# Performance work log

Hardware: AMD Instinct MI355X
Metric: run time of the kernel (lower is better)

The kernel has to match this reference:

```python
import jax, jax.numpy as jnp
import numpy as np

B, T, I, H, O = 128, 1024, 512, 1024, 512
LN_EPS = 1e-5

def _linear_params(key, out_dim, in_dim):
    k1, k2 = jax.random.split(key)
    bound = 1.0 / np.sqrt(in_dim)
    W = jax.random.uniform(k1, (out_dim, in_dim), jnp.float32, -bound, bound)
    b = jax.random.uniform(k2, (out_dim,), jnp.float32, -bound, bound)
    return W, b

def setup_inputs() -> dict:
    key = jax.random.key(0)
    ks = jax.random.split(key, 10)
    x = jax.random.normal(ks[0], (B, T, I), jnp.float32)
    Wir, bir = _linear_params(ks[1], H, I)
    Whr, bhr = _linear_params(ks[2], H, H)
    Wiz, biz = _linear_params(ks[3], H, I)
    Whz, bhz = _linear_params(ks[4], H, H)
    Win, bin_ = _linear_params(ks[5], H, I)
    Whn, bhn = _linear_params(ks[6], H, H)
    Wskip, bskip = _linear_params(ks[7], H, I)
    gamma = jnp.ones((H,), jnp.float32)
    beta = jnp.zeros((H,), jnp.float32)
    Wout, bout = _linear_params(ks[8], O, H)
    return dict(x=x, Wir=Wir, bir=bir, Whr=Whr, bhr=bhr, Wiz=Wiz, biz=biz,
                Whz=Whz, bhz=bhz, Win=Win, bin_=bin_, Whn=Whn, bhn=bhn,
                Wskip=Wskip, bskip=bskip, gamma=gamma, beta=beta,
                Wout=Wout, bout=bout)

def reference(x, Wir, bir, Whr, bhr, Wiz, biz, Whz, bhz, Win, bin_, Whn, bhn,
              Wskip, bskip, gamma, beta, Wout, bout):
    # Precompute input-side projections in one batched GEMM each (same math as per-step Linear).
    rx = jnp.einsum('bti,hi->bth', x, Wir) + bir  # (B,T,H)
    zx = jnp.einsum('bti,hi->bth', x, Wiz) + biz
    nx = jnp.einsum('bti,hi->bth', x, Win) + bin_

    def step(h, inp):
        rx_t, zx_t, nx_t = inp
        r = jax.nn.sigmoid(rx_t + h @ Whr.T + bhr)
        z = jax.nn.sigmoid(zx_t + h @ Whz.T + bhz)
        n = jnp.tanh(nx_t + r * (h @ Whn.T + bhn))
        h_new = (1.0 - z) * n + z * h
        return h_new, h_new

    h0 = jnp.zeros((x.shape[0], Whr.shape[0]), x.dtype)
    xs = (jnp.swapaxes(rx, 0, 1), jnp.swapaxes(zx, 0, 1), jnp.swapaxes(nx, 0, 1))
    _, hs = jax.lax.scan(step, h0, xs)  # hs: (T,B,H)
    hs = jnp.swapaxes(hs, 0, 1)  # (B,T,H)

    skip = jnp.einsum('bti,hi->bth', x, Wskip) + bskip
    combined = hs + skip
    mu = jnp.mean(combined, axis=-1, keepdims=True)
    var = jnp.var(combined, axis=-1, keepdims=True)
    normed = (combined - mu) * jax.lax.rsqrt(var + LN_EPS) * gamma + beta
    out = jnp.einsum('bth,oh->bto', normed, Wout) + bout  # (B,T,O)
    return out
```

## Files before the change

kernel.cpp:

```cpp
#include <hip/hip_runtime.h>

#define T_DIM 1024
#define B_DIM 128
#define I_DIM 512
#define H_DIM 1024
#define O_DIM 512
#define TC 64
#define NCHUNK (T_DIM / TC)

typedef _Float16 half8 __attribute__((ext_vector_type(8)));
typedef _Float16 half4v __attribute__((ext_vector_type(4)));
typedef float floatx4 __attribute__((ext_vector_type(4)));
typedef unsigned int uint4v __attribute__((ext_vector_type(4)));

__device__ __forceinline__ void gload_lds16(const void* g, void* l) {
  __builtin_amdgcn_global_load_lds(
      (const __attribute__((address_space(1))) void*)g,
      (__attribute__((address_space(3))) void*)l, 16, 0, 0);
}

__device__ __forceinline__ float sigmoidf_(float x) {
  return 1.f / (1.f + __expf(-x));
}
__device__ __forceinline__ float tanhf_(float x) {
  float e = __expf(fminf(-2.f * x, 60.f));
  return (1.f - e) / (1.f + e);
}

__global__ __launch_bounds__(256) void k_cvt(const float* __restrict__ s,
                                             _Float16* __restrict__ d, int n4) {
  int i = blockIdx.x * 256 + threadIdx.x;
  if (i < n4) {
    float4 v = ((const float4*)s)[i];
    half4v h = {(_Float16)v.x, (_Float16)v.y, (_Float16)v.z, (_Float16)v.w};
    ((half4v*)d)[i] = h;
  }
}

__global__ __launch_bounds__(256) void k_cvt_x(const float* __restrict__ x,
                                               _Float16* __restrict__ x16, int t0) {
  int i = blockIdx.x * 256 + threadIdx.x;
  int i4 = i & 127;
  int row = i >> 7;
  int b = row & 127, tl = row >> 7;
  float4 v = ((const float4*)(x + ((size_t)b * T_DIM + t0 + tl) * I_DIM))[i4];
  half4v h = {(_Float16)v.x, (_Float16)v.y, (_Float16)v.z, (_Float16)v.w};
  ((half4v*)(x16 + (size_t)row * I_DIM))[i4] = h;
}

__global__ __launch_bounds__(256) void build_bcat(const float* __restrict__ a,
                                                  const float* __restrict__ b,
                                                  const float* __restrict__ c,
                                                  const float* __restrict__ d,
                                                  float* __restrict__ o) {
  int i = blockIdx.x * 256 + threadIdx.x;
  if (i < 4096) {
    const float* p = (i < 1024) ? a : (i < 2048) ? b : (i < 3072) ? c : d;
    o[i] = p[i & 1023];
  }
}

template <int MODE>
__global__ __launch_bounds__(256) void gemm_f16(
    const _Float16* __restrict__ A, const _Float16* __restrict__ B,
    const float* __restrict__ bias, _Float16* __restrict__ C16,
    float* __restrict__ C32, int M, int N, int K, int t0) {
  __shared__ __align__(16) _Float16 As[128 * 64];
  __shared__ __align__(16) _Float16 Bs[128 * 64];
  const int tid = threadIdx.x, lane = tid & 63, wv = tid >> 6;
  const int wm = wv >> 1, wn = wv & 1;
  const int lj = lane & 15, lk = lane >> 4;
  const size_t rowA0 = (size_t)blockIdx.y * 128, colB0 = (size_t)blockIdx.x * 128;
  floatx4 acc[4][4] = {};
  for (int kb = 0; kb < K; kb += 64) {
    __syncthreads();
#pragma unroll
    for (int i = 0; i < 4; ++i) {
      int q = i * 256 + tid;
      int r = q >> 3, c = q & 7;
      gload_lds16(A + (rowA0 + r) * (size_t)K + kb + c * 8, As + (size_t)(i * 4 + wv) * 512);
    }
#pragma unroll
    for (int i = 0; i < 4; ++i) {
      int q = i * 256 + tid;
      int r = q >> 3, c = q & 7;
      gload_lds16(B + (colB0 + r) * (size_t)K + kb + c * 8, Bs + (size_t)(i * 4 + wv) * 512);
    }
    __syncthreads();
#pragma unroll
    for (int ks = 0; ks < 2; ++ks) {
      half8 af[4], bf[4];
#pragma unroll
      for (int am = 0; am < 4; ++am)
        af[am] = *(const half8*)(As + (wm * 64 + am * 16 + lj) * 64 + ks * 32 + lk * 8);
#pragma unroll
      for (int bn = 0; bn < 4; ++bn)
        bf[bn] = *(const half8*)(Bs + (wn * 64 + bn * 16 + lj) * 64 + ks * 32 + lk * 8);
#pragma unroll
      for (int am = 0; am < 4; ++am)
#pragma unroll
        for (int bn = 0; bn < 4; ++bn)
          acc[am][bn] = __builtin_amdgcn_mfma_f32_16x16x32_f16(af[am], bf[bn], acc[am][bn], 0, 0, 0);
    }
  }
#pragma unroll
  for (int am = 0; am < 4; ++am)
#pragma unroll
    for (int bn = 0; bn < 4; ++bn)
#pragma unroll
      for (int rr = 0; rr < 4; ++rr) {
        size_t grow = rowA0 + wm * 64 + am * 16 + lk * 4 + rr;
        size_t gcol = colB0 + wn * 64 + bn * 16 + lj;
        float v = acc[am][bn][rr] + bias[gcol];
        if constexpr (MODE == 0) {
          C16[grow * (size_t)N + gcol] = (_Float16)v;
        } else {
          size_t tl = grow >> 7, b = grow & 127;
          C32[b * (size_t)(T_DIM * O_DIM) + (t0 + tl) * (size_t)O_DIM + gcol] = v;
        }
      }
}

__global__ __launch_bounds__(384) void scan_kernel(
    const _Float16* __restrict__ rznx,
    const _Float16* __restrict__ Whcat,
    const float* __restrict__ bhr, const float* __restrict__ bhz,
    const float* __restrict__ bhn,
    _Float16* __restrict__ h16,
    float* __restrict__ h32,
    _Float16* __restrict__ hs16,
    int* __restrict__ flags,
    int chunk) {
  __shared__ __align__(16) _Float16 hlds[16 * 1024];
  __shared__ float exch[2][2][16 * 17];
  __shared__ __align__(16) _Float16 hout[16][32];
  const int tid = threadIdx.x, lane = tid & 63, wv = tid >> 6;
  const int g = wv % 3, jh = wv / 3;
  const int bg = blockIdx.x & 7, js = blockIdx.x >> 3;
  const int b0 = bg * 16;
  const int jbase = js * 32 + jh * 16;
  const int lj = lane & 15, lk = lane >> 4;
  const int jcol = jbase + lj;

  half8 wf[32];
  {
    const _Float16* wb = Whcat + ((size_t)g * 1024 + jcol) * 1024 + lk * 8;
#pragma unroll
    for (int ks = 0; ks < 32; ++ks) wf[ks] = *(const half8*)(wb + ks * 32);
  }
  const float* bh = (g == 0) ? bhr : (g == 1) ? bhz : bhn;
  const float biasg = bh[jcol];
  float hown[4];
  if (g == 1) {
#pragma unroll
    for (int r = 0; r < 4; ++r) hown[r] = h32[(size_t)(b0 + lk * 4 + r) * 1024 + jcol];
  }
  int cur = 0;
  for (int t = 0; t < TC; ++t) {
    const int gs = chunk * TC + t;
    const _Float16* xg = rznx + ((size_t)t * 128 + b0) * 4096 + g * 1024 + jcol;
    float xv[4];
#pragma unroll
    for (int r = 0; r < 4; ++r) xv[r] = (float)xg[(size_t)(lk * 4 + r) * 4096];
    float nxv[4];
    if (g == 1) {
#pragma unroll
      for (int r = 0; r < 4; ++r)
        nxv[r] = (float)rznx[((size_t)t * 128 + b0 + lk * 4 + r) * 4096 + 2048 + jcol];
    }
    if (tid < 256) {
      const _Float16* hsrc = h16 + (size_t)cur * (128 * 1024) + (size_t)b0 * 1024;
      uint4v vv[8];
      const char* ap[8];
#pragma unroll
      for (int i = 0; i < 8; ++i) {
        int q = tid + i * 256;
        int b = q >> 7, c = q & 127;
        ap[i] = (const char*)(hsrc + b * 1024 + c * 8);
      }
#pragma unroll
      for (int i = 0; i < 8; ++i)
        asm volatile("global_load_dwordx4 %0, %1, off sc0 sc1"
                     : "=v"(vv[i]) : "v"(ap[i]));
      asm volatile("s_waitcnt vmcnt(0)" ::: "memory");
#pragma unroll
      for (int i = 0; i < 8; ++i) {
        int q = tid + i * 256;
        int b = q >> 7, c = q & 127;
        *(uint4v*)((char*)hlds + b * 2048 + ((c ^ (b & 7)) * 16)) = vv[i];
      }
    }
    __syncthreads();
    floatx4 acc = {0.f, 0.f, 0.f, 0.f};
#pragma unroll
    for (int ks = 0; ks < 32; ++ks) {
      int c = ks * 4 + lk;
      int b = lj;
      half8 af = *(const half8*)((const char*)hlds + b * 2048 + ((c ^ (b & 7)) * 16));
      acc = __builtin_amdgcn_mfma_f32_16x16x32_f16(af, wf[ks], acc, 0, 0, 0);
    }
    float zv[4] = {0.f, 0.f, 0.f, 0.f};
    if (g == 0) {
#pragma unroll
      for (int r = 0; r < 4; ++r)
        exch[jh][0][(lk * 4 + r) * 17 + lj] = sigmoidf_(acc[r] + biasg + xv[r]);
    } else if (g == 2) {
#pragma unroll
      for (int r = 0; r < 4; ++r)
        exch[jh][1][(lk * 4 + r) * 17 + lj] = acc[r] + biasg;
    } else {
#pragma unroll
      for (int r = 0; r < 4; ++r) zv[r] = sigmoidf_(acc[r] + biasg + xv[r]);
    }
    __syncthreads();
    if (g == 1) {
#pragma unroll
      for (int r = 0; r < 4; ++r) {
        float rr = exch[jh][0][(lk * 4 + r) * 17 + lj];
        float np = exch[jh][1][(lk * 4 + r) * 17 + lj];
        float n = tanhf_(nxv[r] + rr * np);
        float hn = (1.f - zv[r]) * n + zv[r] * hown[r];
        hown[r] = hn;
        hout[lk * 4 + r][jh * 16 + lj] = (_Float16)hn;
      }
    }
    __syncthreads();
    if (wv == 0) {
      int row = lane >> 2, c = lane & 3;
      uint4v hv = *(const uint4v*)((const char*)hout + row * 64 + c * 16);
      char* p1 = (char*)(h16 + (size_t)(cur ^ 1) * (128 * 1024) +
                         (size_t)(b0 + row) * 1024 + js * 32 + c * 8);
      asm volatile("global_store_dwordx4 %0, %1, off sc0 sc1"
                   :: "v"(p1), "v"(hv) : "memory");
      _Float16* p2 = hs16 + ((size_t)t * 128 + b0 + row) * 1024 + js * 32 + c * 8;
      *(uint4v*)p2 = hv;
      asm volatile("s_waitcnt vmcnt(0)" ::: "memory");
      if (lane == 0) {
        int* fp = flags + ((size_t)bg * 32 + js) * 32;
        int val = gs + 1;
        asm volatile("global_store_dword %0, %1, off sc0 sc1"
                     :: "v"(fp), "v"(val) : "memory");
      }
    } else if (wv == 5) {
      const int* fp = flags + ((size_t)bg * 32 + (lane & 31)) * 32;
      const int target = gs + 1;
      int spin = 0;
      while (true) {
        int v;
        asm volatile("global_load_dword %0, %1, off sc0 sc1\n\ts_waitcnt vmcnt(0)"
                     : "=v"(v) : "v"(fp) : "memory");
        if (__all(v >= target)) break;
        __builtin_amdgcn_s_sleep(1);
        if (++spin > (1 << 17)) break;
      }
    }
    __syncthreads();
    cur ^= 1;
  }
  if (g == 1) {
#pragma unroll
    for (int r = 0; r < 4; ++r) h32[(size_t)(b0 + lk * 4 + r) * 1024 + jcol] = hown[r];
  }
}

__global__ __launch_bounds__(256) void ln_kernel(
    const _Float16* __restrict__ hs, const _Float16* __restrict__ rz,
    const float* __restrict__ gamma, const float* __restrict__ beta,
    _Float16* __restrict__ outp) {
  const int row = blockIdx.x, tid = threadIdx.x;
  const int lane = tid & 63, wv = tid >> 6;
  half4v hv = *(const half4v*)(hs + (size_t)row * 1024 + tid * 4);
  half4v sv = *(const half4v*)(rz + (size_t)row * 4096 + 3072 + tid * 4);
  float v[4];
  float s = 0.f, s2 = 0.f;
#pragma unroll
  for (int j = 0; j < 4; ++j) {
    v[j] = (float)hv[j] + (float)sv[j];
    s += v[j];
    s2 += v[j] * v[j];
  }
#pragma unroll
  for (int o = 32; o > 0; o >>= 1) {
    s += __shfl_xor(s, o, 64);
    s2 += __shfl_xor(s2, o, 64);
  }
  __shared__ float ps[4][2];
  if (lane == 0) { ps[wv][0] = s; ps[wv][1] = s2; }
  __syncthreads();
  s = ps[0][0] + ps[1][0] + ps[2][0] + ps[3][0];
  s2 = ps[0][1] + ps[1][1] + ps[2][1] + ps[3][1];
  const float mu = s * (1.f / 1024.f);
  const float var = s2 * (1.f / 1024.f) - mu * mu;
  const float rstd = rsqrtf(var + 1e-5f);
  half4v ov;
#pragma unroll
  for (int j = 0; j < 4; ++j)
    ov[j] = (_Float16)((v[j] - mu) * rstd * gamma[tid * 4 + j] + beta[tid * 4 + j]);
  *(half4v*)(outp + (size_t)row * 1024 + tid * 4) = ov;
}

extern "C" void kernel_launch(void* const* d_in, const int* in_sizes, int n_in,
                              void* d_out, int out_size, void* d_ws, size_t ws_size,
                              hipStream_t stream) {
  const float* x     = (const float*)d_in[0];
  const float* Wir   = (const float*)d_in[1];
  const float* bir   = (const float*)d_in[2];
  const float* Whr   = (const float*)d_in[3];
  const float* bhr   = (const float*)d_in[4];
  const float* Wiz   = (const float*)d_in[5];
  const float* biz   = (const float*)d_in[6];
  const float* Whz   = (const float*)d_in[7];
  const float* bhz   = (const float*)d_in[8];
  const float* Win   = (const float*)d_in[9];
  const float* bin_  = (const float*)d_in[10];
  const float* Whn   = (const float*)d_in[11];
  const float* bhn   = (const float*)d_in[12];
  const float* Wskip = (const float*)d_in[13];
  const float* bskip = (const float*)d_in[14];
  const float* gamma = (const float*)d_in[15];
  const float* beta  = (const float*)d_in[16];
  const float* Wout  = (const float*)d_in[17];
  const float* bout  = (const float*)d_in[18];
  float* out = (float*)d_out;

  char* ws = (char*)d_ws;
  size_t off = 0;
  auto alloc = [&](size_t bytes) -> char* {
    char* p = ws + off;
    off += (bytes + 255) & ~(size_t)255;
    return p;
  };
  _Float16* x16    = (_Float16*)alloc((size_t)TC * 128 * 512 * 2);
  _Float16* Wcat   = (_Float16*)alloc((size_t)4096 * 512 * 2);
  _Float16* Whcat  = (_Float16*)alloc((size_t)3072 * 1024 * 2);
  _Float16* Wout16 = (_Float16*)alloc((size_t)512 * 1024 * 2);
  float*    bcat   = (float*)alloc(4096 * 4);
  _Float16* rznx   = (_Float16*)alloc((size_t)TC * 128 * 4096 * 2);
  _Float16* h16    = (_Float16*)alloc((size_t)2 * 128 * 1024 * 2);
  float*    h32    = (float*)alloc((size_t)128 * 1024 * 4);
  _Float16* hs16   = (_Float16*)alloc((size_t)TC * 128 * 1024 * 2);
  _Float16* normed = (_Float16*)alloc((size_t)TC * 128 * 1024 * 2);
  int*      flags  = (int*)alloc(8 * 32 * 32 * sizeof(int));

  k_cvt<<<512, 256, 0, stream>>>(Wir, Wcat + 0 * 524288, 131072);
  k_cvt<<<512, 256, 0, stream>>>(Wiz, Wcat + 1 * 524288, 131072);
  k_cvt<<<512, 256, 0, stream>>>(Win, Wcat + 2 * 524288, 131072);
  k_cvt<<<512, 256, 0, stream>>>(Wskip, Wcat + 3 * 524288, 131072);
  k_cvt<<<1024, 256, 0, stream>>>(Whr, Whcat + 0 * 1048576, 262144);
  k_cvt<<<1024, 256, 0, stream>>>(Whz, Whcat + 1 * 1048576, 262144);
  k_cvt<<<1024, 256, 0, stream>>>(Whn, Whcat + 2 * 1048576, 262144);
  k_cvt<<<512, 256, 0, stream>>>(Wout, Wout16, 131072);
  build_bcat<<<16, 256, 0, stream>>>(bir, biz, bin_, bskip, bcat);
  hipMemsetAsync(h16, 0, (size_t)2 * 128 * 1024 * 2, stream);
  hipMemsetAsync(h32, 0, (size_t)128 * 1024 * 4, stream);
  hipMemsetAsync(flags, 0, 8 * 32 * 32 * sizeof(int), stream);

  for (int c = 0; c < NCHUNK; ++c) {
    int t0 = c * TC;
    k_cvt_x<<<(TC * 128 * 512 / 4) / 256, 256, 0, stream>>>(x, x16, t0);
    gemm_f16<0><<<dim3(4096 / 128, TC * 128 / 128), 256, 0, stream>>>(
        x16, Wcat, bcat, rznx, nullptr, TC * 128, 4096, 512, 0);
    scan_kernel<<<256, 384, 0, stream>>>(rznx, Whcat, bhr, bhz, bhn, h16, h32, hs16, flags, c);
    ln_kernel<<<TC * 128, 256, 0, stream>>>(hs16, rznx, gamma, beta, normed);
    gemm_f16<1><<<dim3(512 / 128, TC * 128 / 128), 256, 0, stream>>>(
        normed, Wout16, bout, nullptr, out, TC * 128, 512, 1024, t0);
  }
}
```

Measured before the change: 5.329 ms.

## Overlap recurrent scan with input GEMM, layernorm and output GEMM of adjacent chunks

Fuses the per-chunk scan with the input projection of the next chunk, the layernorm of the previous chunk and the output GEMM of the chunk before that. Blocks 256 to 511 do this side work while blocks 0 to 255 run the latency-bound recurrence. The x conversion is folded into the input GEMM, and the skip add moves into the scan so layernorm reads a single tensor. This needs double-buffered workspace and assumes 512 co-resident blocks, because the scan spins on flags across blocks. The side work may also compete with the scan for CU resources.

```diff
diff --git a/kernel.cpp b/kernel.cpp
--- a/kernel.cpp
+++ b/kernel.cpp
@@ -35,17 +35,6 @@
     half4v h = {(_Float16)v.x, (_Float16)v.y, (_Float16)v.z, (_Float16)v.w};
     ((half4v*)d)[i] = h;
   }
-}
-
-__global__ __launch_bounds__(256) void k_cvt_x(const float* __restrict__ x,
-                                               _Float16* __restrict__ x16, int t0) {
-  int i = blockIdx.x * 256 + threadIdx.x;
-  int i4 = i & 127;
-  int row = i >> 7;
-  int b = row & 127, tl = row >> 7;
-  float4 v = ((const float4*)(x + ((size_t)b * T_DIM + t0 + tl) * I_DIM))[i4];
-  half4v h = {(_Float16)v.x, (_Float16)v.y, (_Float16)v.z, (_Float16)v.w};
-  ((half4v*)(x16 + (size_t)row * I_DIM))[i4] = h;
 }
 
 __global__ __launch_bounds__(256) void build_bcat(const float* __restrict__ a,
@@ -60,243 +49,386 @@
   }
 }
 
-template <int MODE>
-__global__ __launch_bounds__(256) void gemm_f16(
-    const _Float16* __restrict__ A, const _Float16* __restrict__ B,
-    const float* __restrict__ bias, _Float16* __restrict__ C16,
-    float* __restrict__ C32, int M, int N, int K, int t0) {
-  __shared__ __align__(16) _Float16 As[128 * 64];
-  __shared__ __align__(16) _Float16 Bs[128 * 64];
-  const int tid = threadIdx.x, lane = tid & 63, wv = tid >> 6;
-  const int wm = wv >> 1, wn = wv & 1;
+__device__ __forceinline__ void gemm_in_tile(
+    const float* __restrict__ x, const _Float16* __restrict__ Wcat,
+    const float* __restrict__ bias, _Float16* __restrict__ rz_dst,
+    _Float16* __restrict__ skip_dst, int t0, int bx, int by, int tid,
+    _Float16* As, _Float16* Bs) {
+  const bool act = tid < 256;
+  const int lane = tid & 63, wv = tid >> 6;
+  const int wm = (wv >> 1) & 1, wn = wv & 1;
   const int lj = lane & 15, lk = lane >> 4;
-  const size_t rowA0 = (size_t)blockIdx.y * 128, colB0 = (size_t)blockIdx.x * 128;
+  const size_t rowA0 = (size_t)by * 128, colB0 = (size_t)bx * 128;
   floatx4 acc[4][4] = {};
-  for (int kb = 0; kb < K; kb += 64) {
+  for (int kb = 0; kb < I_DIM; kb += 64) {
     __syncthreads();
-#pragma unroll
-    for (int i = 0; i < 4; ++i) {
-      int q = i * 256 + tid;
-      int r = q >> 3, c = q & 7;
-      gload_lds16(A + (rowA0 + r) * (size_t)K + kb + c * 8, As + (size_t)(i * 4 + wv) * 512);
-    }
-#pragma unroll
-    for (int i = 0; i < 4; ++i) {
-      int q = i * 256 + tid;
-      int r = q >> 3, c = q & 7;
-      gload_lds16(B + (colB0 + r) * (size_t)K + kb + c * 8, Bs + (size_t)(i * 4 + wv) * 512);
+    if (act) {
+      float4 av[8];
+#pragma unroll
+      for (int i = 0; i < 8; ++i) {
+        int u = i * 256 + tid;
+        int r = u >> 4, f4 = u & 15;
+        size_t grow = rowA0 + r;
+        size_t b = grow & 127, tl = grow >> 7;
+        av[i] = *(const float4*)(x + (b * T_DIM + t0 + tl) * I_DIM + kb + f4 * 4);
+      }
+#pragma unroll
+      for (int i = 0; i < 4; ++i) {
+        int q = i * 256 + tid;
+        int r = q >> 3, cc = q & 7;
+        gload_lds16(Wcat + (colB0 + r) * (size_t)I_DIM + kb + cc * 8,
+                    Bs + (size_t)(i * 4 + wv) * 512);
+      }
+#pragma unroll
+      for (int i = 0; i < 8; ++i) {
+        int u = i * 256 + tid;
+        int r = u >> 4, f4 = u & 15;
+        half4v h = {(_Float16)av[i].x, (_Float16)av[i].y, (_Float16)av[i].z,
+                    (_Float16)av[i].w};
+        *(half4v*)(As + r * 64 + f4 * 4) = h;
+      }
     }
     __syncthreads();
-#pragma unroll
-    for (int ks = 0; ks < 2; ++ks) {
-      half8 af[4], bf[4];
-#pragma unroll
-      for (int am = 0; am < 4; ++am)
-        af[am] = *(const half8*)(As + (wm * 64 + am * 16 + lj) * 64 + ks * 32 + lk * 8);
+    if (act) {
+#pragma unroll
+      for (int ks = 0; ks < 2; ++ks) {
+        half8 af[4], bf[4];
+#pragma unroll
+        for (int am = 0; am < 4; ++am)
+          af[am] = *(const half8*)(As + (wm * 64 + am * 16 + lj) * 64 + ks * 32 + lk * 8);
+#pragma unroll
+        for (int bn = 0; bn < 4; ++bn)
+          bf[bn] = *(const half8*)(Bs + (wn * 64 + bn * 16 + lj) * 64 + ks * 32 + lk * 8);
+#pragma unroll
+        for (int am = 0; am < 4; ++am)
+#pragma unroll
+          for (int bn = 0; bn < 4; ++bn)
+            acc[am][bn] =
+                __builtin_amdgcn_mfma_f32_16x16x32_f16(af[am], bf[bn], acc[am][bn], 0, 0, 0);
+      }
+    }
+  }
+  if (act) {
+#pragma unroll
+    for (int am = 0; am < 4; ++am)
 #pragma unroll
       for (int bn = 0; bn < 4; ++bn)
-        bf[bn] = *(const half8*)(Bs + (wn * 64 + bn * 16 + lj) * 64 + ks * 32 + lk * 8);
-#pragma unroll
-      for (int am = 0; am < 4; ++am)
+#pragma unroll
+        for (int rr = 0; rr < 4; ++rr) {
+          size_t grow = rowA0 + wm * 64 + am * 16 + lk * 4 + rr;
+          int gcol = (int)colB0 + wn * 64 + bn * 16 + lj;
+          float v = acc[am][bn][rr] + bias[gcol];
+          if (gcol < 3072) rz_dst[grow * 3072 + gcol] = (_Float16)v;
+          else skip_dst[grow * 1024 + (gcol - 3072)] = (_Float16)v;
+        }
+  }
+}
+
+__device__ __forceinline__ void gemm_out_tile(
+    const _Float16* __restrict__ A, const _Float16* __restrict__ Bw,
+    const float* __restrict__ bias, float* __restrict__ C32, int t0, int bx,
+    int by, int tid, _Float16* As, _Float16* Bs) {
+  const bool act = tid < 256;
+  const int lane = tid & 63, wv = tid >> 6;
+  const int wm = (wv >> 1) & 1, wn = wv & 1;
+  const int lj = lane & 15, lk = lane >> 4;
+  const size_t rowA0 = (size_t)by * 128, colB0 = (size_t)bx * 128;
+  floatx4 acc[4][4] = {};
+  for (int kb = 0; kb < H_DIM; kb += 64) {
+    __syncthreads();
+    if (act) {
+#pragma unroll
+      for (int i = 0; i < 4; ++i) {
+        int q = i * 256 + tid;
+        int r = q >> 3, cc = q & 7;
+        gload_lds16(A + (rowA0 + r) * (size_t)H_DIM + kb + cc * 8,
+                    As + (size_t)(i * 4 + wv) * 512);
+      }
+#pragma unroll
+      for (int i = 0; i < 4; ++i) {
+        int q = i * 256 + tid;
+        int r = q >> 3, cc = q & 7;
+        gload_lds16(Bw + (colB0 + r) * (size_t)H_DIM + kb + cc * 8,
+                    Bs + (size_t)(i * 4 + wv) * 512);
+      }
+    }
+    __syncthreads();
+    if (act) {
+#pragma unroll
+      for (int ks = 0; ks < 2; ++ks) {
+        half8 af[4], bf[4];
+#pragma unroll
+        for (int am = 0; am < 4; ++am)
+          af[am] = *(const half8*)(As + (wm * 64 + am * 16 + lj) * 64 + ks * 32 + lk * 8);
 #pragma unroll
         for (int bn = 0; bn < 4; ++bn)
-          acc[am][bn] = __builtin_amdgcn_mfma_f32_16x16x32_f16(af[am], bf[bn], acc[am][bn], 0, 0, 0);
-    }
-  }
-#pragma unroll
-  for (int am = 0; am < 4; ++am)
-#pragma unroll
-    for (int bn = 0; bn < 4; ++bn)
-#pragma unroll
-      for (int rr = 0; rr < 4; ++rr) {
-        size_t grow = rowA0 + wm * 64 + am * 16 + lk * 4 + rr;
-        size_t gcol = colB0 + wn * 64 + bn * 16 + lj;
-        float v = acc[am][bn][rr] + bias[gcol];
-        if constexpr (MODE == 0) {
-          C16[grow * (size_t)N + gcol] = (_Float16)v;
-        } else {
+          bf[bn] = *(const half8*)(Bs + (wn * 64 + bn * 16 + lj) * 64 + ks * 32 + lk * 8);
+#pragma unroll
+        for (int am = 0; am < 4; ++am)
+#pragma unroll
+          for (int bn = 0; bn < 4; ++bn)
+            acc[am][bn] =
+                __builtin_amdgcn_mfma_f32_16x16x32_f16(af[am], bf[bn], acc[am][bn], 0, 0, 0);
+      }
+    }
+  }
+  if (act) {
+#pragma unroll
+    for (int am = 0; am < 4; ++am)
+#pragma unroll
+      for (int bn = 0; bn < 4; ++bn)
+#pragma unroll
+        for (int rr = 0; rr < 4; ++rr) {
+          size_t grow = rowA0 + wm * 64 + am * 16 + lk * 4 + rr;
+          size_t gcol = colB0 + wn * 64 + bn * 16 + lj;
           size_t tl = grow >> 7, b = grow & 127;
-          C32[b * (size_t)(T_DIM * O_DIM) + (t0 + tl) * (size_t)O_DIM + gcol] = v;
-        }
-      }
-}
-
-__global__ __launch_bounds__(384) void scan_kernel(
-    const _Float16* __restrict__ rznx,
+          C32[b * (size_t)(T_DIM * O_DIM) + (t0 + tl) * (size_t)O_DIM + gcol] =
+              acc[am][bn][rr] + bias[gcol];
+        }
+  }
+}
+
+__device__ __forceinline__ void ln_one_row(int row, const _Float16* __restrict__ hs,
+                                           const float* __restrict__ gamma,
+                                           const float* __restrict__ beta,
+                                           _Float16* __restrict__ outp, int tid,
+                                           float* ps) {
+  const bool act = tid < 256;
+  const int lane = tid & 63, wv = tid >> 6;
+  float v[4];
+  float s = 0.f, s2 = 0.f;
+  if (act) {
+    half4v hv = *(const half4v*)(hs + (size_t)row * 1024 + tid * 4);
+#pragma unroll
+    for (int j = 0; j < 4; ++j) {
+      v[j] = (float)hv[j];
+      s += v[j];
+      s2 += v[j] * v[j];
+    }
+#pragma unroll
+    for (int o = 32; o > 0; o >>= 1) {
+      s += __shfl_xor(s, o, 64);
+      s2 += __shfl_xor(s2, o, 64);
+    }
+    if (lane == 0) { ps[wv * 2] = s; ps[wv * 2 + 1] = s2; }
+  }
+  __syncthreads();
+  if (act) {
+    s = ps[0] + ps[2] + ps[4] + ps[6];
+    s2 = ps[1] + ps[3] + ps[5] + ps[7];
+    const float mu = s * (1.f / 1024.f);
+    const float var = s2 * (1.f / 1024.f) - mu * mu;
+    const float rstd = rsqrtf(var + 1e-5f);
+    half4v ov;
+#pragma unroll
+    for (int j = 0; j < 4; ++j)
+      ov[j] = (_Float16)((v[j] - mu) * rstd * gamma[tid * 4 + j] + beta[tid * 4 + j]);
+    *(half4v*)(outp + (size_t)row * 1024 + tid * 4) = ov;
+  }
+  __syncthreads();
+}
+
+__global__ __launch_bounds__(256) void gemm_in_k(
+    const float* __restrict__ x, const _Float16* __restrict__ Wcat,
+    const float* __restrict__ bcat, _Float16* __restrict__ rz,
+    _Float16* __restrict__ skip, int t0) {
+  __shared__ __align__(16) char sm[32768];
+  gemm_in_tile(x, Wcat, bcat, rz, skip, t0, blockIdx.x, blockIdx.y, threadIdx.x,
+               (_Float16*)sm, (_Float16*)(sm + 16384));
+}
+
+__global__ __launch_bounds__(256) void gemm_out_k(
+    const _Float16* __restrict__ A, const _Float16* __restrict__ Bw,
+    const float* __restrict__ bias, float* __restrict__ C32, int t0) {
+  __shared__ __align__(16) char sm[32768];
+  gemm_out_tile(A, Bw, bias, C32, t0, blockIdx.x, blockIdx.y, threadIdx.x,
+                (_Float16*)sm, (_Float16*)(sm + 16384));
+}
+
+__global__ __launch_bounds__(256) void ln_k(const _Float16* __restrict__ hs,
+                                            const float* __restrict__ gamma,
+                                            const float* __restrict__ beta,
+                                            _Float16* __restrict__ normed) {
+  __shared__ float ps[8];
+  ln_one_row(blockIdx.x, hs, gamma, beta, normed, threadIdx.x, ps);
+}
+
+__global__ __launch_bounds__(384, 3) void fused_k(
+    const _Float16* __restrict__ rznx_s,
+    const _Float16* __restrict__ skip_s,
     const _Float16* __restrict__ Whcat,
     const float* __restrict__ bhr, const float* __restrict__ bhz,
     const float* __restrict__ bhn,
-    _Float16* __restrict__ h16,
-    float* __restrict__ h32,
-    _Float16* __restrict__ hs16,
-    int* __restrict__ flags,
-    int chunk) {
-  __shared__ __align__(16) _Float16 hlds[16 * 1024];
-  __shared__ float exch[2][2][16 * 17];
-  __shared__ __align__(16) _Float16 hout[16][32];
-  const int tid = threadIdx.x, lane = tid & 63, wv = tid >> 6;
-  const int g = wv % 3, jh = wv / 3;
-  const int bg = blockIdx.x & 7, js = blockIdx.x >> 3;
-  const int b0 = bg * 16;
-  const int jbase = js * 32 + jh * 16;
-  const int lj = lane & 15, lk = lane >> 4;
-  const int jcol = jbase + lj;
-
-  half8 wf[32];
-  {
-    const _Float16* wb = Whcat + ((size_t)g * 1024 + jcol) * 1024 + lk * 8;
-#pragma unroll
-    for (int ks = 0; ks < 32; ++ks) wf[ks] = *(const half8*)(wb + ks * 32);
-  }
-  const float* bh = (g == 0) ? bhr : (g == 1) ? bhz : bhn;
-  const float biasg = bh[jcol];
-  float hown[4];
-  if (g == 1) {
-#pragma unroll
-    for (int r = 0; r < 4; ++r) hown[r] = h32[(size_t)(b0 + lk * 4 + r) * 1024 + jcol];
-  }
-  int cur = 0;
-  for (int t = 0; t < TC; ++t) {
-    const int gs = chunk * TC + t;
-    const _Float16* xg = rznx + ((size_t)t * 128 + b0) * 4096 + g * 1024 + jcol;
-    float xv[4];
-#pragma unroll
-    for (int r = 0; r < 4; ++r) xv[r] = (float)xg[(size_t)(lk * 4 + r) * 4096];
-    float nxv[4];
+    _Float16* __restrict__ h16, float* __restrict__ h32,
+    _Float16* __restrict__ hs16_s,
+    int* __restrict__ flags, int chunk,
+    const float* __restrict__ x, const _Float16* __restrict__ Wcat,
+    const float* __restrict__ bcat, _Float16* __restrict__ rznx_n,
+    _Float16* __restrict__ skip_n, int do_gin, int t0_gin,
+    const _Float16* __restrict__ hs16_p, const float* __restrict__ gamma,
+    const float* __restrict__ beta, _Float16* __restrict__ normed_p, int do_ln,
+    const _Float16* __restrict__ normed_pp, const _Float16* __restrict__ Wout16,
+    const float* __restrict__ bout, float* __restrict__ outp, int do_gout,
+    int t0_gout) {
+  __shared__ __align__(16) char smem[38400];
+  const int tid = threadIdx.x;
+
+  if (blockIdx.x < 256) {
+    _Float16* hlds = (_Float16*)smem;
+    float* exch = (float*)(smem + 32768);
+    _Float16* hout = (_Float16*)(smem + 37376);
+    const int lane = tid & 63, wv = tid >> 6;
+    const int g = wv % 3, jh = wv / 3;
+    const int bg = blockIdx.x & 7, js = blockIdx.x >> 3;
+    const int b0 = bg * 16;
+    const int jbase = js * 32 + jh * 16;
+    const int lj = lane & 15, lk = lane >> 4;
+    const int jcol = jbase + lj;
+
+    half8 wf[32];
+    {
+      const _Float16* wb = Whcat + ((size_t)g * 1024 + jcol) * 1024 + lk * 8;
+#pragma unroll
+      for (int ks = 0; ks < 32; ++ks) wf[ks] = *(const half8*)(wb + ks * 32);
+    }
+    const float* bh = (g == 0) ? bhr : (g == 1) ? bhz : bhn;
+    const float biasg = bh[jcol];
+    float hown[4];
     if (g == 1) {
 #pragma unroll
       for (int r = 0; r < 4; ++r)
-        nxv[r] = (float)rznx[((size_t)t * 128 + b0 + lk * 4 + r) * 4096 + 2048 + jcol];
-    }
-    if (tid < 256) {
-      const _Float16* hsrc = h16 + (size_t)cur * (128 * 1024) + (size_t)b0 * 1024;
-      uint4v vv[8];
-      const char* ap[8];
-#pragma unroll
-      for (int i = 0; i < 8; ++i) {
-        int q = tid + i * 256;
-        int b = q >> 7, c = q & 127;
-        ap[i] = (const char*)(hsrc + b * 1024 + c * 8);
-      }
-#pragma unroll
-      for (int i = 0; i < 8; ++i)
-        asm volatile("global_load_dwordx4 %0, %1, off sc0 sc1"
-                     : "=v"(vv[i]) : "v"(ap[i]));
-      asm volatile("s_waitcnt vmcnt(0)" ::: "memory");
-#pragma unroll
-      for (int i = 0; i < 8; ++i) {
-        int q = tid + i * 256;
-        int b = q >> 7, c = q & 127;
-        *(uint4v*)((char*)hlds + b * 2048 + ((c ^ (b & 7)) * 16)) = vv[i];
-      }
-    }
+        hown[r] = h32[(size_t)(b0 + lk * 4 + r) * 1024 + jcol];
+    }
+    int cur = 0;
+    for (int t = 0; t < TC; ++t) {
+      const int gs = chunk * TC + t;
+      const _Float16* xg = rznx_s + ((size_t)t * 128 + b0) * 3072 + g * 1024 + jcol;
+      float xv[4];
+#pragma unroll
+      for (int r = 0; r < 4; ++r) xv[r] = (float)xg[(size_t)(lk * 4 + r) * 3072];
+      float nxv[4], skv[4];
+      if (g == 1) {
+#pragma unroll
+        for (int r = 0; r < 4; ++r) {
+          nxv[r] = (float)rznx_s[((size_t)t * 128 + b0 + lk * 4 + r) * 3072 + 2048 + jcol];
+          skv[r] = (float)skip_s[((size_t)t * 128 + b0 + lk * 4 + r) * 1024 + jcol];
+        }
+      }
+      if (tid < 256) {
+        const _Float16* hsrc = h16 + (size_t)cur * (128 * 1024) + (size_t)b0 * 1024;
+        uint4v vv[8];
+        const char* ap[8];
+#pragma unroll
+        for (int i = 0; i < 8; ++i) {
+          int q = tid + i * 256;
+          int b = q >> 7, c = q & 127;
+          ap[i] = (const char*)(hsrc + b * 1024 + c * 8);
+        }
+#pragma unroll
+        for (int i = 0; i < 8; ++i)
+          asm volatile("global_load_dwordx4 %0, %1, off sc0 sc1"
+                       : "=v"(vv[i]) : "v"(ap[i]));
+        asm volatile("s_waitcnt vmcnt(0)" ::: "memory");
+#pragma unroll
+        for (int i = 0; i < 8; ++i) {
+          int q = tid + i * 256;
+          int b = q >> 7, c = q & 127;
+          *(uint4v*)((char*)hlds + b * 2048 + ((c ^ (b & 7)) * 16)) = vv[i];
+        }
+      }
+      __syncthreads();
+      floatx4 acc = {0.f, 0.f, 0.f, 0.f};
+#pragma unroll
+      for (int ks = 0; ks < 32; ++ks) {
+        int c = ks * 4 + lk;
+        int b = lj;
+        half8 af = *(const half8*)((const char*)hlds + b * 2048 + ((c ^ (b & 7)) * 16));
+        acc = __builtin_amdgcn_mfma_f32_16x16x32_f16(af, wf[ks], acc, 0, 0, 0);
+      }
+      float zv[4] = {0.f, 0.f, 0.f, 0.f};
+      if (g == 0) {
+#pragma unroll
+        for (int r = 0; r < 4; ++r)
+          exch[(jh * 2 + 0) * 272 + (lk * 4 + r) * 17 + lj] =
+              sigmoidf_(acc[r] + biasg + xv[r]);
+      } else if (g == 2) {
+#pragma unroll
+        for (int r = 0; r < 4; ++r)
+          exch[(jh * 2 + 1) * 272 + (lk * 4 + r) * 17 + lj] = acc[r] + biasg;
+      } else {
+#pragma unroll
+        for (int r = 0; r < 4; ++r) zv[r] = sigmoidf_(acc[r] + biasg + xv[r]);
+      }
+      __syncthreads();
+      if (g == 1) {
+#pragma unroll
+        for (int r = 0; r < 4; ++r) {
+          float rr = exch[(jh * 2 + 0) * 272 + (lk * 4 + r) * 17 + lj];
+          float np = exch[(jh * 2 + 1) * 272 + (lk * 4 + r) * 17 + lj];
+          float n = tanhf_(nxv[r] + rr * np);
+          float hn = (1.f - zv[r]) * n + zv[r] * hown[r];
+          hown[r] = hn;
+          hout[(lk * 4 + r) * 32 + jh * 16 + lj] = (_Float16)hn;
+          hs16_s[((size_t)t * 128 + b0 + lk * 4 + r) * 1024 + jcol] =
+              (_Float16)(hn + skv[r]);
+        }
+      }
+      __syncthreads();
+      if (wv == 0) {
+        int row = lane >> 2, c = lane & 3;
+        uint4v hv = *(const uint4v*)((const char*)hout + row * 64 + c * 16);
+        char* p1 = (char*)(h16 + (size_t)(cur ^ 1) * (128 * 1024) +
+                           (size_t)(b0 + row) * 1024 + js * 32 + c * 8);
+        asm volatile("global_store_dwordx4 %0, %1, off sc0 sc1"
+                     :: "v"(p1), "v"(hv) : "memory");
+        asm volatile("s_waitcnt vmcnt(0)" ::: "memory");
+        if (lane == 0) {
+          int* fp = flags + ((size_t)bg * 32 + js) * 32;
+          int val = gs + 1;
+          asm volatile("global_store_dword %0, %1, off sc0 sc1"
+                       :: "v"(fp), "v"(val) : "memory");
+        }
+      } else if (wv == 5) {
+        const int* fp = flags + ((size_t)bg * 32 + (lane & 31)) * 32;
+        const int target = gs + 1;
+        int spin = 0;
+        while (true) {
+          int v;
+          asm volatile("global_load_dword %0, %1, off sc0 sc1\n\ts_waitcnt vmcnt(0)"
+                       : "=v"(v) : "v"(fp) : "memory");
+          if (__all(v >= target)) break;
+          __builtin_amdgcn_s_sleep(1);
+          if (++spin > (1 << 18)) break;
+        }
+      }
+      __syncthreads();
+      cur ^= 1;
+    }
+    if (g == 1) {
+#pragma unroll
+      for (int r = 0; r < 4; ++r)
+        h32[(size_t)(b0 + lk * 4 + r) * 1024 + jcol] = hown[r];
+    }
+    return;
+  }
+
+  const int w = blockIdx.x - 256;
+  _Float16* As = (_Float16*)smem;
+  _Float16* Bs = (_Float16*)(smem + 16384);
+  float* ps = (float*)(smem + 32768);
+  if (do_gin) {
+    for (int tau = w; tau < 2048; tau += 256)
+      gemm_in_tile(x, Wcat, bcat, rznx_n, skip_n, t0_gin, tau & 31, tau >> 5, tid,
+                   As, Bs);
+  }
+  if (do_ln) {
+    for (int row = w; row < TC * 128; row += 256)
+      ln_one_row(row, hs16_p, gamma, beta, normed_p, tid, ps);
+  }
+  if (do_gout) {
     __syncthreads();
-    floatx4 acc = {0.f, 0.f, 0.f, 0.f};
-#pragma unroll
-    for (int ks = 0; ks < 32; ++ks) {
-      int c = ks * 4 + lk;
-      int b = lj;
-      half8 af = *(const half8*)((const char*)hlds + b * 2048 + ((c ^ (b & 7)) * 16));
-      acc = __builtin_amdgcn_mfma_f32_16x16x32_f16(af, wf[ks], acc, 0, 0, 0);
-    }
-    float zv[4] = {0.f, 0.f, 0.f, 0.f};
-    if (g == 0) {
-#pragma unroll
-      for (int r = 0; r < 4; ++r)
-        exch[jh][0][(lk * 4 + r) * 17 + lj] = sigmoidf_(acc[r] + biasg + xv[r]);
-    } else if (g == 2) {
-#pragma unroll
-      for (int r = 0; r < 4; ++r)
-        exch[jh][1][(lk * 4 + r) * 17 + lj] = acc[r] + biasg;
-    } else {
-#pragma unroll
-      for (int r = 0; r < 4; ++r) zv[r] = sigmoidf_(acc[r] + biasg + xv[r]);
-    }
-    __syncthreads();
-    if (g == 1) {
-#pragma unroll
-      for (int r = 0; r < 4; ++r) {
-        float rr = exch[jh][0][(lk * 4 + r) * 17 + lj];
-        float np = exch[jh][1][(lk * 4 + r) * 17 + lj];
-        float n = tanhf_(nxv[r] + rr * np);
-        float hn = (1.f - zv[r]) * n + zv[r] * hown[r];
-        hown[r] = hn;
-        hout[lk * 4 + r][jh * 16 + lj] = (_Float16)hn;
-      }
-    }
-    __syncthreads();
-    if (wv == 0) {
-      int row = lane >> 2, c = lane & 3;
-      uint4v hv = *(const uint4v*)((const char*)hout + row * 64 + c * 16);
-      char* p1 = (char*)(h16 + (size_t)(cur ^ 1) * (128 * 1024) +
-                         (size_t)(b0 + row) * 1024 + js * 32 + c * 8);
-      asm volatile("global_store_dwordx4 %0, %1, off sc0 sc1"
-                   :: "v"(p1), "v"(hv) : "memory");
-      _Float16* p2 = hs16 + ((size_t)t * 128 + b0 + row) * 1024 + js * 32 + c * 8;
-      *(uint4v*)p2 = hv;
-      asm volatile("s_waitcnt vmcnt(0)" ::: "memory");
-      if (lane == 0) {
-        int* fp = flags + ((size_t)bg * 32 + js) * 32;
-        int val = gs + 1;
-        asm volatile("global_store_dword %0, %1, off sc0 sc1"
-                     :: "v"(fp), "v"(val) : "memory");
-      }
-    } else if (wv == 5) {
-      const int* fp = flags + ((size_t)bg * 32 + (lane & 31)) * 32;
-      const int target = gs + 1;
-      int spin = 0;
-      while (true) {
-        int v;
-        asm volatile("global_load_dword %0, %1, off sc0 sc1\n\ts_waitcnt vmcnt(0)"
-                     : "=v"(v) : "v"(fp) : "memory");
-        if (__all(v >= target)) break;
-        __builtin_amdgcn_s_sleep(1);
-        if (++spin > (1 << 17)) break;
-      }
-    }
-    __syncthreads();
-    cur ^= 1;
-  }
-  if (g == 1) {
-#pragma unroll
-    for (int r = 0; r < 4; ++r) h32[(size_t)(b0 + lk * 4 + r) * 1024 + jcol] = hown[r];
-  }
-}
-
-__global__ __launch_bounds__(256) void ln_kernel(
-    const _Float16* __restrict__ hs, const _Float16* __restrict__ rz,
-    const float* __restrict__ gamma, const float* __restrict__ beta,
-    _Float16* __restrict__ outp) {
-  const int row = blockIdx.x, tid = threadIdx.x;
-  const int lane = tid & 63, wv = tid >> 6;
-  half4v hv = *(const half4v*)(hs + (size_t)row * 1024 + tid * 4);
-  half4v sv = *(const half4v*)(rz + (size_t)row * 4096 + 3072 + tid * 4);
-  float v[4];
-  float s = 0.f, s2 = 0.f;
-#pragma unroll
-  for (int j = 0; j < 4; ++j) {
-    v[j] = (float)hv[j] + (float)sv[j];
-    s += v[j];
-    s2 += v[j] * v[j];
-  }
-#pragma unroll
-  for (int o = 32; o > 0; o >>= 1) {
-    s += __shfl_xor(s, o, 64);
-    s2 += __shfl_xor(s2, o, 64);
-  }
-  __shared__ float ps[4][2];
-  if (lane == 0) { ps[wv][0] = s; ps[wv][1] = s2; }
-  __syncthreads();
-  s = ps[0][0] + ps[1][0] + ps[2][0] + ps[3][0];
-  s2 = ps[0][1] + ps[1][1] + ps[2][1] + ps[3][1];
-  const float mu = s * (1.f / 1024.f);
-  const float var = s2 * (1.f / 1024.f) - mu * mu;
-  const float rstd = rsqrtf(var + 1e-5f);
-  half4v ov;
-#pragma unroll
-  for (int j = 0; j < 4; ++j)
-    ov[j] = (_Float16)((v[j] - mu) * rstd * gamma[tid * 4 + j] + beta[tid * 4 + j]);
-  *(half4v*)(outp + (size_t)row * 1024 + tid * 4) = ov;
+    gemm_out_tile(normed_pp, Wout16, bout, outp, t0_gout, w & 3, w >> 2, tid, As, Bs);
+  }
 }
 
 extern "C" void kernel_launch(void* const* d_in, const int* in_sizes, int n_in,
@@ -330,17 +462,30 @@
     off += (bytes + 255) & ~(size_t)255;
     return p;
   };
-  _Float16* x16    = (_Float16*)alloc((size_t)TC * 128 * 512 * 2);
   _Float16* Wcat   = (_Float16*)alloc((size_t)4096 * 512 * 2);
   _Float16* Whcat  = (_Float16*)alloc((size_t)3072 * 1024 * 2);
   _Float16* Wout16 = (_Float16*)alloc((size_t)512 * 1024 * 2);
   float*    bcat   = (float*)alloc(4096 * 4);
-  _Float16* rznx   = (_Float16*)alloc((size_t)TC * 128 * 4096 * 2);
   _Float16* h16    = (_Float16*)alloc((size_t)2 * 128 * 1024 * 2);
   float*    h32    = (float*)alloc((size_t)128 * 1024 * 4);
-  _Float16* hs16   = (_Float16*)alloc((size_t)TC * 128 * 1024 * 2);
-  _Float16* normed = (_Float16*)alloc((size_t)TC * 128 * 1024 * 2);
   int*      flags  = (int*)alloc(8 * 32 * 32 * sizeof(int));
+  _Float16* rznx0  = (_Float16*)alloc((size_t)TC * 128 * 3072 * 2);
+  _Float16* skip0  = (_Float16*)alloc((size_t)TC * 128 * 1024 * 2);
+  _Float16* hs0    = (_Float16*)alloc((size_t)TC * 128 * 1024 * 2);
+  _Float16* norm0  = (_Float16*)alloc((size_t)TC * 128 * 1024 * 2);
+  size_t shallow_end = off;
+  _Float16* rznx1  = (_Float16*)alloc((size_t)TC * 128 * 3072 * 2);
+  _Float16* skip1  = (_Float16*)alloc((size_t)TC * 128 * 1024 * 2);
+  _Float16* hs1    = (_Float16*)alloc((size_t)TC * 128 * 1024 * 2);
+  _Float16* norm1  = (_Float16*)alloc((size_t)TC * 128 * 1024 * 2);
+  size_t deep_end = off;
+  const bool deep = ws_size >= deep_end;
+  (void)shallow_end;
+
+  _Float16* rznxA[2] = {rznx0, rznx1};
+  _Float16* skipA[2] = {skip0, skip1};
+  _Float16* hsA[2]   = {hs0, hs1};
+  _Float16* normA[2] = {norm0, norm1};
 
   k_cvt<<<512, 256, 0, stream>>>(Wir, Wcat + 0 * 524288, 131072);
   k_cvt<<<512, 256, 0, stream>>>(Wiz, Wcat + 1 * 524288, 131072);
@@ -355,14 +500,32 @@
   hipMemsetAsync(h32, 0, (size_t)128 * 1024 * 4, stream);
   hipMemsetAsync(flags, 0, 8 * 32 * 32 * sizeof(int), stream);
 
-  for (int c = 0; c < NCHUNK; ++c) {
-    int t0 = c * TC;
-    k_cvt_x<<<(TC * 128 * 512 / 4) / 256, 256, 0, stream>>>(x, x16, t0);
-    gemm_f16<0><<<dim3(4096 / 128, TC * 128 / 128), 256, 0, stream>>>(
-        x16, Wcat, bcat, rznx, nullptr, TC * 128, 4096, 512, 0);
-    scan_kernel<<<256, 384, 0, stream>>>(rznx, Whcat, bhr, bhz, bhn, h16, h32, hs16, flags, c);
-    ln_kernel<<<TC * 128, 256, 0, stream>>>(hs16, rznx, gamma, beta, normed);
-    gemm_f16<1><<<dim3(512 / 128, TC * 128 / 128), 256, 0, stream>>>(
-        normed, Wout16, bout, nullptr, out, TC * 128, 512, 1024, t0);
-  }
-}
+  if (deep) {
+    gemm_in_k<<<dim3(32, 64), 256, 0, stream>>>(x, Wcat, bcat, rznxA[0], skipA[0], 0);
+    for (int c = 0; c < NCHUNK; ++c) {
+      int gin = (c + 1 < NCHUNK) ? 1 : 0;
+      int lnn = (c >= 1) ? 1 : 0;
+      int got = (c >= 2) ? 1 : 0;
+      fused_k<<<512, 384, 0, stream>>>(
+          rznxA[c & 1], skipA[c & 1], Whcat, bhr, bhz, bhn, h16, h32, hsA[c & 1],
+          flags, c,
+          x, Wcat, bcat, rznxA[(c + 1) & 1], skipA[(c + 1) & 1], gin, (c + 1) * TC,
+          hsA[(c - 1) & 1], gamma, beta, normA[(c - 1) & 1], lnn,
+          normA[c & 1], Wout16, bout, out, got, (c - 2) * TC);
+    }
+    ln_k<<<TC * 128, 256, 0, stream>>>(hsA[1], gamma, beta, normA[1]);
+    gemm_out_k<<<dim3(4, 64), 256, 0, stream>>>(normA[0], Wout16, bout, out, 14 * TC);
+    gemm_out_k<<<dim3(4, 64), 256, 0, stream>>>(normA[1], Wout16, bout, out, 15 * TC);
+  } else {
+    for (int c = 0; c < NCHUNK; ++c) {
+      gemm_in_k<<<dim3(32, 64), 256, 0, stream>>>(x, Wcat, bcat, rznx0, skip0, c * TC);
+      fused_k<<<256, 384, 0, stream>>>(
+          rznx0, skip0, Whcat, bhr, bhz, bhn, h16, h32, hs0, flags, c,
+          x, Wcat, bcat, rznx0, skip0, 0, 0,
+          hs0, gamma, beta, norm0, 0,
+          norm0, Wout16, bout, out, 0, 0);
+      ln_k<<<TC * 128, 256, 0, stream>>>(hs0, gamma, beta, norm0);
+      gemm_out_k<<<dim3(4, 64), 256, 0, stream>>>(norm0, Wout16, bout, out, c * TC);
+    }
+  }
+}
```

New measurement: 13.83 ms. 2.59x slower.

## Fuse x conversion into input GEMM and skip-add into scan

Applied to the files above, without the earlier changes.

The input GEMM now reads fp32 x directly and converts it to fp16 in registers before the LDS store, which removes the separate k_cvt_x kernel and its x16 buffer. The GEMM output is split into a 3072-wide rz/nx buffer and a separate skip buffer. The scan kernel adds the skip term when it writes hs16, so the LN kernel no longer reads it. The spin-wait in the scan now busy-polls before it starts sleeping. In exchange, the A tile is loaded synchronously through registers instead of global_load_lds, and the scan does extra per-step loads and scattered fp16 stores.

```diff
diff --git a/kernel.cpp b/kernel.cpp
--- a/kernel.cpp
+++ b/kernel.cpp
@@ -35,17 +35,6 @@
     half4v h = {(_Float16)v.x, (_Float16)v.y, (_Float16)v.z, (_Float16)v.w};
     ((half4v*)d)[i] = h;
   }
-}
-
-__global__ __launch_bounds__(256) void k_cvt_x(const float* __restrict__ x,
-                                               _Float16* __restrict__ x16, int t0) {
-  int i = blockIdx.x * 256 + threadIdx.x;
-  int i4 = i & 127;
-  int row = i >> 7;
-  int b = row & 127, tl = row >> 7;
-  float4 v = ((const float4*)(x + ((size_t)b * T_DIM + t0 + tl) * I_DIM))[i4];
-  half4v h = {(_Float16)v.x, (_Float16)v.y, (_Float16)v.z, (_Float16)v.w};
-  ((half4v*)(x16 + (size_t)row * I_DIM))[i4] = h;
 }
 
 __global__ __launch_bounds__(256) void build_bcat(const float* __restrict__ a,
@@ -60,11 +49,10 @@
   }
 }
 
-template <int MODE>
-__global__ __launch_bounds__(256) void gemm_f16(
-    const _Float16* __restrict__ A, const _Float16* __restrict__ B,
-    const float* __restrict__ bias, _Float16* __restrict__ C16,
-    float* __restrict__ C32, int M, int N, int K, int t0) {
+__global__ __launch_bounds__(256) void gemm_in_k(
+    const float* __restrict__ x, const _Float16* __restrict__ Wcat,
+    const float* __restrict__ bias, _Float16* __restrict__ rz_dst,
+    _Float16* __restrict__ skip_dst, int t0) {
   __shared__ __align__(16) _Float16 As[128 * 64];
   __shared__ __align__(16) _Float16 Bs[128 * 64];
   const int tid = threadIdx.x, lane = tid & 63, wv = tid >> 6;
@@ -72,19 +60,89 @@
   const int lj = lane & 15, lk = lane >> 4;
   const size_t rowA0 = (size_t)blockIdx.y * 128, colB0 = (size_t)blockIdx.x * 128;
   floatx4 acc[4][4] = {};
-  for (int kb = 0; kb < K; kb += 64) {
-    __syncthreads();
+  for (int kb = 0; kb < I_DIM; kb += 64) {
+    __syncthreads();
+    float4 av[8];
+#pragma unroll
+    for (int i = 0; i < 8; ++i) {
+      int u = i * 256 + tid;
+      int r = u >> 4, f4 = u & 15;
+      size_t grow = rowA0 + r;
+      size_t b = grow & 127, tl = grow >> 7;
+      av[i] = *(const float4*)(x + (b * T_DIM + t0 + tl) * I_DIM + kb + f4 * 4);
+    }
 #pragma unroll
     for (int i = 0; i < 4; ++i) {
       int q = i * 256 + tid;
-      int r = q >> 3, c = q & 7;
-      gload_lds16(A + (rowA0 + r) * (size_t)K + kb + c * 8, As + (size_t)(i * 4 + wv) * 512);
-    }
+      int r = q >> 3, cc = q & 7;
+      gload_lds16(Wcat + (colB0 + r) * (size_t)I_DIM + kb + cc * 8,
+                  Bs + (size_t)(i * 4 + wv) * 512);
+    }
+#pragma unroll
+    for (int i = 0; i < 8; ++i) {
+      int u = i * 256 + tid;
+      int r = u >> 4, f4 = u & 15;
+      half4v h = {(_Float16)av[i].x, (_Float16)av[i].y, (_Float16)av[i].z,
+                  (_Float16)av[i].w};
+      *(half4v*)(As + r * 64 + f4 * 4) = h;
+    }
+    __syncthreads();
+#pragma unroll
+    for (int ks = 0; ks < 2; ++ks) {
+      half8 af[4], bf[4];
+#pragma unroll
+      for (int am = 0; am < 4; ++am)
+        af[am] = *(const half8*)(As + (wm * 64 + am * 16 + lj) * 64 + ks * 32 + lk * 8);
+#pragma unroll
+      for (int bn = 0; bn < 4; ++bn)
+        bf[bn] = *(const half8*)(Bs + (wn * 64 + bn * 16 + lj) * 64 + ks * 32 + lk * 8);
+#pragma unroll
+      for (int am = 0; am < 4; ++am)
+#pragma unroll
+        for (int bn = 0; bn < 4; ++bn)
+          acc[am][bn] =
+              __builtin_amdgcn_mfma_f32_16x16x32_f16(af[am], bf[bn], acc[am][bn], 0, 0, 0);
+    }
+  }
+#pragma unroll
+  for (int am = 0; am < 4; ++am)
+#pragma unroll
+    for (int bn = 0; bn < 4; ++bn)
+#pragma unroll
+      for (int rr = 0; rr < 4; ++rr) {
+        size_t grow = rowA0 + wm * 64 + am * 16 + lk * 4 + rr;
+        int gcol = (int)colB0 + wn * 64 + bn * 16 + lj;
+        float v = acc[am][bn][rr] + bias[gcol];
+        if (gcol < 3072) rz_dst[grow * 3072 + gcol] = (_Float16)v;
+        else skip_dst[grow * 1024 + (gcol - 3072)] = (_Float16)v;
+      }
+}
+
+__global__ __launch_bounds__(256) void gemm_out_k(
+    const _Float16* __restrict__ A, const _Float16* __restrict__ Bw,
+    const float* __restrict__ bias, float* __restrict__ C32, int t0) {
+  __shared__ __align__(16) _Float16 As[128 * 64];
+  __shared__ __align__(16) _Float16 Bs[128 * 64];
+  const int tid = threadIdx.x, lane = tid & 63, wv = tid >> 6;
+  const int wm = wv >> 1, wn = wv & 1;
+  const int lj = lane & 15, lk = lane >> 4;
+  const size_t rowA0 = (size_t)blockIdx.y * 128, colB0 = (size_t)blockIdx.x * 128;
+  floatx4 acc[4][4] = {};
+  for (int kb = 0; kb < H_DIM; kb += 64) {
+    __syncthreads();
 #pragma unroll
     for (int i = 0; i < 4; ++i) {
       int q = i * 256 + tid;
-      int r = q >> 3, c = q & 7;
-      gload_lds16(B + (colB0 + r) * (size_t)K + kb + c * 8, Bs + (size_t)(i * 4 + wv) * 512);
+      int r = q >> 3, cc = q & 7;
+      gload_lds16(A + (rowA0 + r) * (size_t)H_DIM + kb + cc * 8,
+                  As + (size_t)(i * 4 + wv) * 512);
+    }
+#pragma unroll
+    for (int i = 0; i < 4; ++i) {
+      int q = i * 256 + tid;
+      int r = q >> 3, cc = q & 7;
+      gload_lds16(Bw + (colB0 + r) * (size_t)H_DIM + kb + cc * 8,
+                  Bs + (size_t)(i * 4 + wv) * 512);
     }
     __syncthreads();
 #pragma unroll
@@ -100,7 +158,8 @@
       for (int am = 0; am < 4; ++am)
 #pragma unroll
         for (int bn = 0; bn < 4; ++bn)
-          acc[am][bn] = __builtin_amdgcn_mfma_f32_16x16x32_f16(af[am], bf[bn], acc[am][bn], 0, 0, 0);
+          acc[am][bn] =
+              __builtin_amdgcn_mfma_f32_16x16x32_f16(af[am], bf[bn], acc[am][bn], 0, 0, 0);
     }
   }
 #pragma unroll
@@ -111,18 +170,15 @@
       for (int rr = 0; rr < 4; ++rr) {
         size_t grow = rowA0 + wm * 64 + am * 16 + lk * 4 + rr;
         size_t gcol = colB0 + wn * 64 + bn * 16 + lj;
-        float v = acc[am][bn][rr] + bias[gcol];
-        if constexpr (MODE == 0) {
-          C16[grow * (size_t)N + gcol] = (_Float16)v;
-        } else {
-          size_t tl = grow >> 7, b = grow & 127;
-          C32[b * (size_t)(T_DIM * O_DIM) + (t0 + tl) * (size_t)O_DIM + gcol] = v;
-        }
+        size_t tl = grow >> 7, b = grow & 127;
+        C32[b * (size_t)(T_DIM * O_DIM) + (t0 + tl) * (size_t)O_DIM + gcol] =
+            acc[am][bn][rr] + bias[gcol];
       }
 }
 
 __global__ __launch_bounds__(384) void scan_kernel(
     const _Float16* __restrict__ rznx,
+    const _Float16* __restrict__ skip,
     const _Float16* __restrict__ Whcat,
     const float* __restrict__ bhr, const float* __restrict__ bhz,
     const float* __restrict__ bhn,
@@ -158,15 +214,17 @@
   int cur = 0;
   for (int t = 0; t < TC; ++t) {
     const int gs = chunk * TC + t;
-    const _Float16* xg = rznx + ((size_t)t * 128 + b0) * 4096 + g * 1024 + jcol;
+    const _Float16* xg = rznx + ((size_t)t * 128 + b0) * 3072 + g * 1024 + jcol;
     float xv[4];
 #pragma unroll
-    for (int r = 0; r < 4; ++r) xv[r] = (float)xg[(size_t)(lk * 4 + r) * 4096];
-    float nxv[4];
+    for (int r = 0; r < 4; ++r) xv[r] = (float)xg[(size_t)(lk * 4 + r) * 3072];
+    float nxv[4], skv[4];
     if (g == 1) {
 #pragma unroll
-      for (int r = 0; r < 4; ++r)
-        nxv[r] = (float)rznx[((size_t)t * 128 + b0 + lk * 4 + r) * 4096 + 2048 + jcol];
+      for (int r = 0; r < 4; ++r) {
+        nxv[r] = (float)rznx[((size_t)t * 128 + b0 + lk * 4 + r) * 3072 + 2048 + jcol];
+        skv[r] = (float)skip[((size_t)t * 128 + b0 + lk * 4 + r) * 1024 + jcol];
+      }
     }
     if (tid < 256) {
       const _Float16* hsrc = h16 + (size_t)cur * (128 * 1024) + (size_t)b0 * 1024;
@@ -222,6 +280,7 @@
         float hn = (1.f - zv[r]) * n + zv[r] * hown[r];
         hown[r] = hn;
         hout[lk * 4 + r][jh * 16 + lj] = (_Float16)hn;
+        hs16[((size_t)t * 128 + b0 + lk * 4 + r) * 1024 + jcol] = (_Float16)(hn + skv[r]);
       }
     }
     __syncthreads();
@@ -232,8 +291,6 @@
                          (size_t)(b0 + row) * 1024 + js * 32 + c * 8);
       asm volatile("global_store_dwordx4 %0, %1, off sc0 sc1"
                    :: "v"(p1), "v"(hv) : "memory");
-      _Float16* p2 = hs16 + ((size_t)t * 128 + b0 + row) * 1024 + js * 32 + c * 8;
-      *(uint4v*)p2 = hv;
       asm volatile("s_waitcnt vmcnt(0)" ::: "memory");
       if (lane == 0) {
         int* fp = flags + ((size_t)bg * 32 + js) * 32;
@@ -250,8 +307,8 @@
         asm volatile("global_load_dword %0, %1, off sc0 sc1\n\ts_waitcnt vmcnt(0)"
                      : "=v"(v) : "v"(fp) : "memory");
         if (__all(v >= target)) break;
-        __builtin_amdgcn_s_sleep(1);
-        if (++spin > (1 << 17)) break;
+        if (++spin > 1024) __builtin_amdgcn_s_sleep(1);
+        if (spin > (1 << 18)) break;
       }
     }
     __syncthreads();
@@ -264,18 +321,16 @@
 }
 
 __global__ __launch_bounds__(256) void ln_kernel(
-    const _Float16* __restrict__ hs, const _Float16* __restrict__ rz,
-    const float* __restrict__ gamma, const float* __restrict__ beta,
-    _Float16* __restrict__ outp) {
+    const _Float16* __restrict__ hs, const float* __restrict__ gamma,
+    const float* __restrict__ beta, _Float16* __restrict__ outp) {
   const int row = blockIdx.x, tid = threadIdx.x;
   const int lane = tid & 63, wv = tid >> 6;
   half4v hv = *(const half4v*)(hs + (size_t)row * 1024 + tid * 4);
-  half4v sv = *(const half4v*)(rz + (size_t)row * 4096 + 3072 + tid * 4);
   float v[4];
   float s = 0.f, s2 = 0.f;
 #pragma unroll
   for (int j = 0; j < 4; ++j) {
-    v[j] = (float)hv[j] + (float)sv[j];
+    v[j] = (float)hv[j];
     s += v[j];
     s2 += v[j] * v[j];
   }
@@ -330,12 +385,12 @@
     off += (bytes + 255) & ~(size_t)255;
     return p;
   };
-  _Float16* x16    = (_Float16*)alloc((size_t)TC * 128 * 512 * 2);
   _Float16* Wcat   = (_Float16*)alloc((size_t)4096 * 512 * 2);
   _Float16* Whcat  = (_Float16*)alloc((size_t)3072 * 1024 * 2);
   _Float16* Wout16 = (_Float16*)alloc((size_t)512 * 1024 * 2);
   float*    bcat   = (float*)alloc(4096 * 4);
-  _Float16* rznx   = (_Float16*)alloc((size_t)TC * 128 * 4096 * 2);
+  _Float16* rznx   = (_Float16*)alloc((size_t)TC * 128 * 3072 * 2);
+  _Float16* skip   = (_Float16*)alloc((size_t)TC * 128 * 1024 * 2);
   _Float16* h16    = (_Float16*)alloc((size_t)2 * 128 * 1024 * 2);
   float*    h32    = (float*)alloc((size_t)128 * 1024 * 4);
   _Float16* hs16   = (_Float16*)alloc((size_t)TC * 128 * 1024 * 2);
@@ -357,12 +412,10 @@
 
   for (int c = 0; c < NCHUNK; ++c) {
     int t0 = c * TC;
-    k_cvt_x<<<(TC * 128 * 512 / 4) / 256, 256, 0, stream>>>(x, x16, t0);
-    gemm_f16<0><<<dim3(4096 / 128, TC * 128 / 128), 256, 0, stream>>>(
-        x16, Wcat, bcat, rznx, nullptr, TC * 128, 4096, 512, 0);
-    scan_kernel<<<256, 384, 0, stream>>>(rznx, Whcat, bhr, bhz, bhn, h16, h32, hs16, flags, c);
-    ln_kernel<<<TC * 128, 256, 0, stream>>>(hs16, rznx, gamma, beta, normed);
-    gemm_f16<1><<<dim3(512 / 128, TC * 128 / 128), 256, 0, stream>>>(
-        normed, Wout16, bout, nullptr, out, TC * 128, 512, 1024, t0);
-  }
-}
+    gemm_in_k<<<dim3(32, 64), 256, 0, stream>>>(x, Wcat, bcat, rznx, skip, t0);
+    scan_kernel<<<256, 384, 0, stream>>>(rznx, skip, Whcat, bhr, bhz, bhn, h16, h32,
+                                         hs16, flags, c);
+    ln_kernel<<<TC * 128, 256, 0, stream>>>(hs16, gamma, beta, normed);
+    gemm_out_k<<<dim3(4, 64), 256, 0, stream>>>(normed, Wout16, bout, out, t0);
+  }
+}
```

After: 6.188 ms. 16.1% more time.
